# Optimization experiments

Hardware: AMD Instinct MI355X
Metric: run time of the kernel (lower is better)

The kernel has to match this reference:

```python
import jax, jax.numpy as jnp
import numpy as np

N, E, F_IN, H, OUT, G = 40000, 640000, 128, 128, 10, 256


def setup_inputs() -> dict:
    key = jax.random.key(0)
    ks = jax.random.split(key, 8)
    x = jax.random.normal(ks[0], (N, F_IN), dtype=jnp.float32)
    edge_index = jax.random.randint(ks[1], (2, E), 0, N, dtype=jnp.int32)
    batch = jnp.sort(jax.random.randint(ks[2], (N,), 0, G, dtype=jnp.int32))
    W1 = jax.random.normal(ks[3], (F_IN, H), dtype=jnp.float32) / np.sqrt(F_IN)
    b1 = jnp.zeros((H,), dtype=jnp.float32)
    W2 = jax.random.normal(ks[4], (H, H), dtype=jnp.float32) / np.sqrt(H)
    b2 = jnp.zeros((H,), dtype=jnp.float32)
    Wfc = jax.random.normal(ks[5], (H, OUT), dtype=jnp.float32) / np.sqrt(H)
    bfc = jnp.zeros((OUT,), dtype=jnp.float32)
    return {"x": x, "edge_index": edge_index, "batch": batch,
            "W1": W1, "b1": b1, "W2": W2, "b2": b2, "Wfc": Wfc, "bfc": bfc}


def _gcn_conv(x, W, b, row, col, num_nodes):
    # x' = D^{-1/2} (A+I) D^{-1/2} (x W) + b   (self-loops already in row/col)
    xw = x @ W                                            # [N, H]
    ones = jnp.ones(row.shape[0], dtype=x.dtype)
    deg = jax.ops.segment_sum(ones, col, num_segments=num_nodes)
    dinv = jnp.where(deg > 0, jax.lax.rsqrt(jnp.maximum(deg, 1.0)), 0.0)
    norm = dinv[row] * dinv[col]                          # [E+N]
    msg = xw[row] * norm[:, None]                         # gather + scale
    return jax.ops.segment_sum(msg, col, num_segments=num_nodes) + b


def reference(x, edge_index, batch, W1, b1, W2, b2, Wfc, bfc):
    num_nodes = x.shape[0]
    loop = jnp.arange(num_nodes, dtype=edge_index.dtype)
    row = jnp.concatenate([edge_index[0], loop])
    col = jnp.concatenate([edge_index[1], loop])

    h = jax.nn.relu(_gcn_conv(x, W1, b1, row, col, num_nodes))
    h = jax.nn.relu(_gcn_conv(h, W2, b2, row, col, num_nodes))

    # global_mean_pool over graph ids
    sums = jax.ops.segment_sum(h, batch, num_segments=G)  # [G, H]
    cnt = jax.ops.segment_sum(jnp.ones(num_nodes, h.dtype), batch, num_segments=G)
    pooled = sums / jnp.maximum(cnt, 1.0)[:, None]

    logits = pooled @ Wfc + bfc                           # [G, OUT]
    return jax.nn.log_softmax(logits, axis=-1)
```

## Files before the change

### kernel.cpp

```cpp
#include <hip/hip_runtime.h>
#include <math.h>

#define H_DIM 128
#define OUT_DIM 10

typedef __attribute__((ext_vector_type(8))) __bf16 bf16x8;
typedef __attribute__((ext_vector_type(8))) unsigned short ushort8;
typedef __attribute__((ext_vector_type(4))) float f32x4;

__device__ inline unsigned short f2bf_rne(float f) {
    unsigned int u = __float_as_uint(f);
    unsigned int r = u + 0x7FFFu + ((u >> 16) & 1u);
    return (unsigned short)(r >> 16);
}
__device__ inline float bf_lo(unsigned int u) { return __uint_as_float(u << 16); }
__device__ inline float bf_hi(unsigned int u) { return __uint_as_float(u & 0xFFFF0000u); }

__global__ __launch_bounds__(256) void hist_kernel(const int* __restrict__ col,
                                                   int* __restrict__ cnt, int E) {
    int e = blockIdx.x * 256 + threadIdx.x;
    if (e < E) atomicAdd(&cnt[col[e]], 1);
}

__global__ __launch_bounds__(256) void scan_phase1(const int* __restrict__ cnt,
                                                   int* __restrict__ blockSums,
                                                   float* __restrict__ dinv, int N) {
    __shared__ int red[256];
    int base = blockIdx.x * 1024;
    int t = threadIdx.x;
    int s = 0;
    for (int i = 0; i < 4; ++i) {
        int idx = base + t * 4 + i;
        if (idx < N) {
            int cv = cnt[idx];
            s += cv;
            dinv[idx] = rsqrtf((float)cv + 1.0f);
        }
    }
    red[t] = s;
    __syncthreads();
    for (int d = 128; d > 0; d >>= 1) {
        if (t < d) red[t] += red[t + d];
        __syncthreads();
    }
    if (t == 0) blockSums[blockIdx.x] = red[0];
}

__global__ __launch_bounds__(256) void scan_phase2(const int* __restrict__ blockSums,
                                                   int* __restrict__ blockOffs,
                                                   int* __restrict__ offs, int B, int N) {
    __shared__ int sh[256];
    int t = threadIdx.x;
    sh[t] = (t < B) ? blockSums[t] : 0;
    __syncthreads();
    for (int d = 1; d < 256; d <<= 1) {
        int v = (t >= d) ? sh[t - d] : 0;
        __syncthreads();
        sh[t] += v;
        __syncthreads();
    }
    if (t < B) blockOffs[t] = (t == 0) ? 0 : sh[t - 1];
    if (t == 255) offs[N] = sh[255];
}

__global__ __launch_bounds__(256) void scan_phase3(const int* __restrict__ cnt,
                                                   const int* __restrict__ blockOffs,
                                                   int* __restrict__ offs,
                                                   int* __restrict__ cursor, int N) {
    __shared__ int red[256];
    int base = blockIdx.x * 1024;
    int t = threadIdx.x;
    int v[4];
    int s = 0;
    for (int i = 0; i < 4; ++i) {
        int idx = base + t * 4 + i;
        v[i] = (idx < N) ? cnt[idx] : 0;
        s += v[i];
    }
    red[t] = s;
    __syncthreads();
    for (int d = 1; d < 256; d <<= 1) {
        int x = (t >= d) ? red[t - d] : 0;
        __syncthreads();
        red[t] += x;
        __syncthreads();
    }
    int run = blockOffs[blockIdx.x] + ((t == 0) ? 0 : red[t - 1]);
    for (int i = 0; i < 4; ++i) {
        int idx = base + t * 4 + i;
        if (idx < N) { offs[idx] = run; cursor[idx] = run; run += v[i]; }
    }
}

__global__ __launch_bounds__(256) void scatter_kernel(const int* __restrict__ row,
                                                      const int* __restrict__ col,
                                                      const float* __restrict__ dinv,
                                                      int* __restrict__ cursor,
                                                      int2* __restrict__ csr, int E) {
    int e = blockIdx.x * 256 + threadIdx.x;
    if (e >= E) return;
    int r = row[e], c = col[e];
    int pos = atomicAdd(&cursor[c], 1);
    int2 p; p.x = r; p.y = __float_as_int(dinv[r] * dinv[c]);
    csr[pos] = p;
}

__global__ __launch_bounds__(256) void wconvert(const float* __restrict__ W1,
                                                const float* __restrict__ W2,
                                                unsigned short* __restrict__ Wt1Hi,
                                                unsigned short* __restrict__ Wt1Lo,
                                                unsigned short* __restrict__ Wt2Hi,
                                                unsigned short* __restrict__ Wt2Lo) {
    int i = blockIdx.x * 256 + threadIdx.x;
    const float* src       = (i < 16384) ? W1    : W2;
    unsigned short* dh     = (i < 16384) ? Wt1Hi : Wt2Hi;
    unsigned short* dl     = (i < 16384) ? Wt1Lo : Wt2Lo;
    int idx = i & 16383;
    int k = idx >> 7, n = idx & 127;
    float v = src[idx];
    unsigned short hb = f2bf_rne(v);
    float hf = __uint_as_float((unsigned int)hb << 16);
    unsigned short lb = f2bf_rne(v - hf);
    dh[n * H_DIM + k] = hb;
    dl[n * H_DIM + k] = lb;
}

__global__ __launch_bounds__(256) void xsplit(const float* __restrict__ X,
                                              unsigned short* __restrict__ Xhi,
                                              unsigned short* __restrict__ Xlo,
                                              int total8) {
    int i = blockIdx.x * 256 + threadIdx.x;
    if (i >= total8) return;
    const float* p = X + (size_t)i * 8;
    f32x4 a = *(const f32x4*)p;
    f32x4 b = *(const f32x4*)(p + 4);
    float v[8] = {a.x, a.y, a.z, a.w, b.x, b.y, b.z, b.w};
    ushort8 h, l;
    #pragma unroll
    for (int j = 0; j < 8; ++j) {
        unsigned short hb = f2bf_rne(v[j]);
        float hf = __uint_as_float((unsigned int)hb << 16);
        h[j] = hb;
        l[j] = f2bf_rne(v[j] - hf);
    }
    *(ushort8*)(Xhi + (size_t)i * 8) = h;
    *(ushort8*)(Xlo + (size_t)i * 8) = l;
}

__global__ __launch_bounds__(256) void gemm_mfma_splitA(const unsigned short* __restrict__ Ahi,
                                                        const unsigned short* __restrict__ Alo,
                                                        const unsigned short* __restrict__ WtHi,
                                                        const unsigned short* __restrict__ WtLo,
                                                        unsigned short* __restrict__ Yb, int N) {
    int lane = threadIdx.x & 63;
    int wv   = threadIdx.x >> 6;
    int m16  = lane & 15;
    int quad = lane >> 4;
    int nodeBase = blockIdx.x * 32;

    f32x4 acc[2][2] = {};

    #pragma unroll
    for (int kt = 0; kt < 4; ++kt) {
        int k0 = kt * 32 + quad * 8;

        ushort8 aHi[2], aLo[2];
        #pragma unroll
        for (int mi = 0; mi < 2; ++mi) {
            int node = nodeBase + mi * 16 + m16;
            if (node >= N) node = N - 1;
            size_t off = (size_t)node * H_DIM + k0;
            aHi[mi] = *(const ushort8*)(Ahi + off);
            aLo[mi] = *(const ushort8*)(Alo + off);
        }

        ushort8 bHi[2], bLo[2];
        #pragma unroll
        for (int ni = 0; ni < 2; ++ni) {
            int n = (wv * 2 + ni) * 16 + m16;
            size_t off = (size_t)n * H_DIM + k0;
            bHi[ni] = *(const ushort8*)(WtHi + off);
            bLo[ni] = *(const ushort8*)(WtLo + off);
        }

        #pragma unroll
        for (int mi = 0; mi < 2; ++mi)
            #pragma unroll
            for (int ni = 0; ni < 2; ++ni) {
                acc[mi][ni] = __builtin_amdgcn_mfma_f32_16x16x32_bf16(
                    __builtin_bit_cast(bf16x8, aHi[mi]),
                    __builtin_bit_cast(bf16x8, bHi[ni]), acc[mi][ni], 0, 0, 0);
                acc[mi][ni] = __builtin_amdgcn_mfma_f32_16x16x32_bf16(
                    __builtin_bit_cast(bf16x8, aLo[mi]),
                    __builtin_bit_cast(bf16x8, bHi[ni]), acc[mi][ni], 0, 0, 0);
                acc[mi][ni] = __builtin_amdgcn_mfma_f32_16x16x32_bf16(
                    __builtin_bit_cast(bf16x8, aHi[mi]),
                    __builtin_bit_cast(bf16x8, bLo[ni]), acc[mi][ni], 0, 0, 0);
            }
    }

    #pragma unroll
    for (int mi = 0; mi < 2; ++mi)
        #pragma unroll
        for (int r = 0; r < 4; ++r) {
            int node = nodeBase + mi * 16 + quad * 4 + r;
            if (node < N) {
                #pragma unroll
                for (int ni = 0; ni < 2; ++ni) {
                    int c = (wv * 2 + ni) * 16 + m16;
                    Yb[(size_t)node * H_DIM + c] = f2bf_rne(acc[mi][ni][r]);
                }
            }
        }
}

__global__ __launch_bounds__(256) void gemm_mfma_bf16A(const unsigned short* __restrict__ Xb,
                                                       const unsigned short* __restrict__ WtHi,
                                                       const unsigned short* __restrict__ WtLo,
                                                       unsigned short* __restrict__ Yb, int N) {
    int lane = threadIdx.x & 63;
    int wv   = threadIdx.x >> 6;
    int m16  = lane & 15;
    int quad = lane >> 4;
    int nodeBase = blockIdx.x * 32;

    f32x4 acc[2][2] = {};

    #pragma unroll
    for (int kt = 0; kt < 4; ++kt) {
        int k0 = kt * 32 + quad * 8;

        ushort8 a[2];
        #pragma unroll
        for (int mi = 0; mi < 2; ++mi) {
            int node = nodeBase + mi * 16 + m16;
            if (node >= N) node = N - 1;
            a[mi] = *(const ushort8*)(Xb + (size_t)node * H_DIM + k0);
        }

        ushort8 bHi[2], bLo[2];
        #pragma unroll
        for (int ni = 0; ni < 2; ++ni) {
            int n = (wv * 2 + ni) * 16 + m16;
            size_t off = (size_t)n * H_DIM + k0;
            bHi[ni] = *(const ushort8*)(WtHi + off);
            bLo[ni] = *(const ushort8*)(WtLo + off);
        }

        #pragma unroll
        for (int mi = 0; mi < 2; ++mi)
            #pragma unroll
            for (int ni = 0; ni < 2; ++ni) {
                acc[mi][ni] = __builtin_amdgcn_mfma_f32_16x16x32_bf16(
                    __builtin_bit_cast(bf16x8, a[mi]),
                    __builtin_bit_cast(bf16x8, bHi[ni]), acc[mi][ni], 0, 0, 0);
                acc[mi][ni] = __builtin_amdgcn_mfma_f32_16x16x32_bf16(
                    __builtin_bit_cast(bf16x8, a[mi]),
                    __builtin_bit_cast(bf16x8, bLo[ni]), acc[mi][ni], 0, 0, 0);
            }
    }

    #pragma unroll
    for (int mi = 0; mi < 2; ++mi)
        #pragma unroll
        for (int r = 0; r < 4; ++r) {
            int node = nodeBase + mi * 16 + quad * 4 + r;
            if (node < N) {
                #pragma unroll
                for (int ni = 0; ni < 2; ++ni) {
                    int c = (wv * 2 + ni) * 16 + m16;
                    Yb[(size_t)node * H_DIM + c] = f2bf_rne(acc[mi][ni][r]);
                }
            }
        }
}

__global__ __launch_bounds__(256) void agg_fused(const unsigned short* __restrict__ XWb,
                                                 const float* __restrict__ dinv,
                                                 const int2* __restrict__ csr,
                                                 const int* __restrict__ offs,
                                                 const float* __restrict__ bias,
                                                 unsigned short* __restrict__ OUTb, int N) {
    int wave = (blockIdx.x * 256 + threadIdx.x) >> 6;
    int lane = threadIdx.x & 63;
    if (wave >= N) return;
    int c = wave;
    int start = offs[c], end = offs[c + 1];
    float dc = dinv[c];
    const unsigned int* XW32 = (const unsigned int*)XWb;

    float ax0, ay0;
    {
        unsigned int u = XW32[(size_t)c * 64 + lane];
        float s = dc * dc;
        ax0 = bf_lo(u) * s; ay0 = bf_hi(u) * s;
    }
    float ax1 = 0.f, ay1 = 0.f, ax2 = 0.f, ay2 = 0.f, ax3 = 0.f, ay3 = 0.f;

    for (int base = start; base < end; base += 64) {
        int m = end - base; if (m > 64) m = 64;
        int2 ce; ce.x = 0; ce.y = 0;
        if (lane < m) ce = csr[base + lane];

        int j = 0;
        for (; j + 3 < m; j += 4) {
            int r0 = __shfl(ce.x, j);     int b0 = __shfl(ce.y, j);
            int r1 = __shfl(ce.x, j + 1); int b1 = __shfl(ce.y, j + 1);
            int r2 = __shfl(ce.x, j + 2); int b2 = __shfl(ce.y, j + 2);
            int r3 = __shfl(ce.x, j + 3); int b3 = __shfl(ce.y, j + 3);
            unsigned int g0 = XW32[(size_t)r0 * 64 + lane];
            unsigned int g1 = XW32[(size_t)r1 * 64 + lane];
            unsigned int g2 = XW32[(size_t)r2 * 64 + lane];
            unsigned int g3 = XW32[(size_t)r3 * 64 + lane];
            float n0 = __int_as_float(b0);
            float n1 = __int_as_float(b1);
            float n2 = __int_as_float(b2);
            float n3 = __int_as_float(b3);
            ax0 += bf_lo(g0) * n0; ay0 += bf_hi(g0) * n0;
            ax1 += bf_lo(g1) * n1; ay1 += bf_hi(g1) * n1;
            ax2 += bf_lo(g2) * n2; ay2 += bf_hi(g2) * n2;
            ax3 += bf_lo(g3) * n3; ay3 += bf_hi(g3) * n3;
        }
        for (; j < m; ++j) {
            int r = __shfl(ce.x, j); int b = __shfl(ce.y, j);
            unsigned int g = XW32[(size_t)r * 64 + lane];
            float nrm = __int_as_float(b);
            ax1 += bf_lo(g) * nrm; ay1 += bf_hi(g) * nrm;
        }
    }
    float ax = (ax0 + ax1) + (ax2 + ax3);
    float ay = (ay0 + ay1) + (ay2 + ay3);
    float2 b = ((const float2*)bias)[lane];
    ax = fmaxf(ax + b.x, 0.f);
    ay = fmaxf(ay + b.y, 0.f);
    unsigned int o = (unsigned int)f2bf_rne(ax) | ((unsigned int)f2bf_rne(ay) << 16);
    ((unsigned int*)(OUTb + (size_t)c * H_DIM))[lane] = o;
}

__global__ __launch_bounds__(256) void pool_partial(const unsigned short* __restrict__ Hb,
                                                    const int* __restrict__ batch,
                                                    float* __restrict__ pooledSum, int N) {
    __shared__ int sb[64];
    int base = blockIdx.x * 64;
    int t = threadIdx.x;
    if (t < 64) {
        int idx = base + t;
        sb[t] = (idx < N) ? batch[idx] : -1;
    }
    __syncthreads();
    int f   = t & 127;
    int sub = t >> 7;
    int n0  = sub * 32;
    float acc = 0.f;
    int curg = -1;
    #pragma unroll 4
    for (int i = 0; i < 32; ++i) {
        int n = base + n0 + i;
        if (n >= N) break;
        int g = sb[n0 + i];
        if (g != curg) {
            if (curg >= 0) atomicAdd(&pooledSum[curg * H_DIM + f], acc);
            acc = 0.f; curg = g;
        }
        acc += __uint_as_float(((unsigned int)Hb[(size_t)n * H_DIM + f]) << 16);
    }
    if (curg >= 0) atomicAdd(&pooledSum[curg * H_DIM + f], acc);
}

__global__ __launch_bounds__(64) void head_kernel(const float* __restrict__ pooledSum,
                                                  const int* __restrict__ batch,
                                                  const float* __restrict__ Wfc,
                                                  const float* __restrict__ bfc,
                                                  float* __restrict__ out, int N) {
    __shared__ float sl[OUT_DIM + 2];
    __shared__ int bounds[2];
    int g = blockIdx.x;
    int j = threadIdx.x;
    if (j < 2) {
        int v = g + j;
        int lo = 0, hi = N;
        while (lo < hi) {
            int mid = (lo + hi) >> 1;
            if (batch[mid] < v) lo = mid + 1; else hi = mid;
        }
        bounds[j] = lo;
    }
    __syncthreads();
    int cnt = bounds[1] - bounds[0];
    float inv = 1.0f / (float)(cnt > 0 ? cnt : 1);
    if (j < OUT_DIM) {
        float acc = 0.f;
        const float* p = pooledSum + g * H_DIM;
        for (int k = 0; k < H_DIM; ++k) acc += p[k] * Wfc[k * OUT_DIM + j];
        sl[j] = acc * inv + bfc[j];
    }
    __syncthreads();
    if (j == 0) {
        float m = sl[0];
        for (int i = 1; i < OUT_DIM; ++i) m = fmaxf(m, sl[i]);
        float s = 0.f;
        for (int i = 0; i < OUT_DIM; ++i) s += expf(sl[i] - m);
        sl[OUT_DIM] = m + logf(s);
    }
    __syncthreads();
    if (j < OUT_DIM) out[g * OUT_DIM + j] = sl[j] - sl[OUT_DIM];
}

extern "C" void kernel_launch(void* const* d_in, const int* in_sizes, int n_in,
                              void* d_out, int out_size, void* d_ws, size_t ws_size,
                              hipStream_t stream) {
    const float* x     = (const float*)d_in[0];
    const int*   ei    = (const int*)  d_in[1];
    const int*   batch = (const int*)  d_in[2];
    const float* W1    = (const float*)d_in[3];
    const float* b1    = (const float*)d_in[4];
    const float* W2    = (const float*)d_in[5];
    const float* b2    = (const float*)d_in[6];
    const float* Wfc   = (const float*)d_in[7];
    const float* bfc   = (const float*)d_in[8];
    float* out = (float*)d_out;

    int N = in_sizes[2];
    int E = in_sizes[1] / 2;
    int G = out_size / OUT_DIM;
    const int* row = ei;
    const int* col = ei + E;

    char* wsb = (char*)d_ws;
    size_t nAlign = (size_t)((N + 256) / 256) * 256;
    int*   cnt    = (int*)wsb;
    int*   offs   = cnt + nAlign;
    int*   cursor = offs + nAlign;
    float* dinv   = (float*)(cursor + nAlign);
    int2*  csr    = (int2*)(dinv + nAlign);
    unsigned short* Xb = (unsigned short*)(csr + E);
    unsigned short* Hb = Xb + (size_t)N * H_DIM;
    float* pooledSum = (float*)(Hb + (size_t)N * H_DIM);
    int* blockSums = (int*)(pooledSum + (size_t)G * H_DIM);
    int* blockOffs = blockSums + 256;
    unsigned short* Wt1Hi = (unsigned short*)(blockOffs + 256);
    unsigned short* Wt1Lo = Wt1Hi + H_DIM * H_DIM;
    unsigned short* Wt2Hi = Wt1Lo + H_DIM * H_DIM;
    unsigned short* Wt2Lo = Wt2Hi + H_DIM * H_DIM;
    unsigned short* Xhi = Wt2Lo + H_DIM * H_DIM;
    unsigned short* Xlo = Xhi + (size_t)N * H_DIM;

    int scanBlocks = (N + 1023) / 1024;
    int total8 = N * H_DIM / 8;

    wconvert<<<128, 256, 0, stream>>>(W1, W2, Wt1Hi, Wt1Lo, Wt2Hi, Wt2Lo);
    xsplit<<<(total8 + 255) / 256, 256, 0, stream>>>(x, Xhi, Xlo, total8);

    hipMemsetAsync(cnt, 0, N * sizeof(int), stream);
    hist_kernel<<<(E + 255) / 256, 256, 0, stream>>>(col, cnt, E);
    scan_phase1<<<scanBlocks, 256, 0, stream>>>(cnt, blockSums, dinv, N);
    scan_phase2<<<1, 256, 0, stream>>>(blockSums, blockOffs, offs, scanBlocks, N);
    scan_phase3<<<scanBlocks, 256, 0, stream>>>(cnt, blockOffs, offs, cursor, N);
    scatter_kernel<<<(E + 255) / 256, 256, 0, stream>>>(row, col, dinv, cursor, csr, E);

    int aggBlocks  = (N + 3) / 4;
    int gemmBlocks = (N + 31) / 32;

    gemm_mfma_splitA<<<gemmBlocks, 256, 0, stream>>>(Xhi, Xlo, Wt1Hi, Wt1Lo, Xb, N);
    agg_fused<<<aggBlocks, 256, 0, stream>>>(Xb, dinv, csr, offs, b1, Hb, N);

    gemm_mfma_bf16A<<<gemmBlocks, 256, 0, stream>>>(Hb, Wt2Hi, Wt2Lo, Xb, N);
    agg_fused<<<aggBlocks, 256, 0, stream>>>(Xb, dinv, csr, offs, b2, Hb, N);

    hipMemsetAsync(pooledSum, 0, (size_t)G * H_DIM * sizeof(float), stream);
    pool_partial<<<(N + 63) / 64, 256, 0, stream>>>(Hb, batch, pooledSum, N);
    head_kernel<<<G, 64, 0, stream>>>(pooledSum, batch, Wfc, bfc, out, N);
}
```

Baseline: 273.6 us.

## Fuse prep kernels, use single-pass decoupled scan, merge memsets

Merges the weight conversion, x hi/lo split and degree histogram into one launch with block-range dispatch. Replaces the three-phase scan with a single-pass chained scan where each block waits on its predecessor's flag. Rearranges the workspace so one memset clears the counts, the pool accumulators and the scan flags. This removes several kernel launches and inter-kernel gaps. It adds a serial spin-wait chain across the roughly 40 scan blocks, which relies on earlier blocks being scheduled first.

```diff
diff --git a/kernel.cpp b/kernel.cpp
--- a/kernel.cpp
+++ b/kernel.cpp
@@ -16,66 +16,77 @@
 __device__ inline float bf_lo(unsigned int u) { return __uint_as_float(u << 16); }
 __device__ inline float bf_hi(unsigned int u) { return __uint_as_float(u & 0xFFFF0000u); }
 
-__global__ __launch_bounds__(256) void hist_kernel(const int* __restrict__ col,
+__global__ __launch_bounds__(256) void prep_kernel(const float* __restrict__ W1,
+                                                   const float* __restrict__ W2,
+                                                   unsigned short* __restrict__ Wt1Hi,
+                                                   unsigned short* __restrict__ Wt1Lo,
+                                                   unsigned short* __restrict__ Wt2Hi,
+                                                   unsigned short* __restrict__ Wt2Lo,
+                                                   const float* __restrict__ X,
+                                                   unsigned short* __restrict__ Xhi,
+                                                   unsigned short* __restrict__ Xlo,
+                                                   int total8, int xb,
+                                                   const int* __restrict__ col,
                                                    int* __restrict__ cnt, int E) {
-    int e = blockIdx.x * 256 + threadIdx.x;
-    if (e < E) atomicAdd(&cnt[col[e]], 1);
-}
-
-__global__ __launch_bounds__(256) void scan_phase1(const int* __restrict__ cnt,
-                                                   int* __restrict__ blockSums,
-                                                   float* __restrict__ dinv, int N) {
+    if (blockIdx.x < 128) {
+        int i = blockIdx.x * 256 + threadIdx.x;
+        const float* src   = (i < 16384) ? W1    : W2;
+        unsigned short* dh = (i < 16384) ? Wt1Hi : Wt2Hi;
+        unsigned short* dl = (i < 16384) ? Wt1Lo : Wt2Lo;
+        int idx = i & 16383;
+        int k = idx >> 7, n = idx & 127;
+        float v = src[idx];
+        unsigned short hb = f2bf_rne(v);
+        float hf = __uint_as_float((unsigned int)hb << 16);
+        unsigned short lb = f2bf_rne(v - hf);
+        dh[n * H_DIM + k] = hb;
+        dl[n * H_DIM + k] = lb;
+    } else if (blockIdx.x < 128 + xb) {
+        int i = (blockIdx.x - 128) * 256 + threadIdx.x;
+        if (i >= total8) return;
+        const float* p = X + (size_t)i * 8;
+        f32x4 a = *(const f32x4*)p;
+        f32x4 b = *(const f32x4*)(p + 4);
+        float v[8] = {a.x, a.y, a.z, a.w, b.x, b.y, b.z, b.w};
+        ushort8 h, l;
+        #pragma unroll
+        for (int j = 0; j < 8; ++j) {
+            unsigned short hb = f2bf_rne(v[j]);
+            float hf = __uint_as_float((unsigned int)hb << 16);
+            h[j] = hb;
+            l[j] = f2bf_rne(v[j] - hf);
+        }
+        *(ushort8*)(Xhi + (size_t)i * 8) = h;
+        *(ushort8*)(Xlo + (size_t)i * 8) = l;
+    } else {
+        int e = (blockIdx.x - 128 - xb) * 256 + threadIdx.x;
+        if (e < E) atomicAdd(&cnt[col[e]], 1);
+    }
+}
+
+__global__ __launch_bounds__(256) void scan_onepass(const int* __restrict__ cnt,
+                                                    int* __restrict__ offs,
+                                                    int* __restrict__ cursor,
+                                                    float* __restrict__ dinv,
+                                                    int* __restrict__ flags,
+                                                    int* __restrict__ incl,
+                                                    int N, int B) {
     __shared__ int red[256];
-    int base = blockIdx.x * 1024;
+    __shared__ int sPrev;
+    int bid = blockIdx.x;
+    int base = bid * 1024;
     int t = threadIdx.x;
+    int v[4];
     int s = 0;
+    #pragma unroll
     for (int i = 0; i < 4; ++i) {
         int idx = base + t * 4 + i;
         if (idx < N) {
             int cv = cnt[idx];
+            v[i] = cv;
             s += cv;
             dinv[idx] = rsqrtf((float)cv + 1.0f);
-        }
-    }
-    red[t] = s;
-    __syncthreads();
-    for (int d = 128; d > 0; d >>= 1) {
-        if (t < d) red[t] += red[t + d];
-        __syncthreads();
-    }
-    if (t == 0) blockSums[blockIdx.x] = red[0];
-}
-
-__global__ __launch_bounds__(256) void scan_phase2(const int* __restrict__ blockSums,
-                                                   int* __restrict__ blockOffs,
-                                                   int* __restrict__ offs, int B, int N) {
-    __shared__ int sh[256];
-    int t = threadIdx.x;
-    sh[t] = (t < B) ? blockSums[t] : 0;
-    __syncthreads();
-    for (int d = 1; d < 256; d <<= 1) {
-        int v = (t >= d) ? sh[t - d] : 0;
-        __syncthreads();
-        sh[t] += v;
-        __syncthreads();
-    }
-    if (t < B) blockOffs[t] = (t == 0) ? 0 : sh[t - 1];
-    if (t == 255) offs[N] = sh[255];
-}
-
-__global__ __launch_bounds__(256) void scan_phase3(const int* __restrict__ cnt,
-                                                   const int* __restrict__ blockOffs,
-                                                   int* __restrict__ offs,
-                                                   int* __restrict__ cursor, int N) {
-    __shared__ int red[256];
-    int base = blockIdx.x * 1024;
-    int t = threadIdx.x;
-    int v[4];
-    int s = 0;
-    for (int i = 0; i < 4; ++i) {
-        int idx = base + t * 4 + i;
-        v[i] = (idx < N) ? cnt[idx] : 0;
-        s += v[i];
+        } else v[i] = 0;
     }
     red[t] = s;
     __syncthreads();
@@ -85,11 +96,26 @@
         red[t] += x;
         __syncthreads();
     }
-    int run = blockOffs[blockIdx.x] + ((t == 0) ? 0 : red[t - 1]);
+    if (t == 0) {
+        int blockTotal = red[255];
+        int prev = 0;
+        if (bid > 0) {
+            while (atomicAdd(&flags[bid - 1], 0) == 0) { }
+            prev = atomicAdd(&incl[bid - 1], 0);
+        }
+        atomicExch(&incl[bid], prev + blockTotal);
+        __threadfence();
+        atomicExch(&flags[bid], 1);
+        sPrev = prev;
+    }
+    __syncthreads();
+    int run = sPrev + ((t == 0) ? 0 : red[t - 1]);
+    #pragma unroll
     for (int i = 0; i < 4; ++i) {
         int idx = base + t * 4 + i;
         if (idx < N) { offs[idx] = run; cursor[idx] = run; run += v[i]; }
     }
+    if (bid == B - 1 && t == 255) offs[N] = run;
 }
 
 __global__ __launch_bounds__(256) void scatter_kernel(const int* __restrict__ row,
@@ -103,48 +129,6 @@
     int pos = atomicAdd(&cursor[c], 1);
     int2 p; p.x = r; p.y = __float_as_int(dinv[r] * dinv[c]);
     csr[pos] = p;
-}
-
-__global__ __launch_bounds__(256) void wconvert(const float* __restrict__ W1,
-                                                const float* __restrict__ W2,
-                                                unsigned short* __restrict__ Wt1Hi,
-                                                unsigned short* __restrict__ Wt1Lo,
-                                                unsigned short* __restrict__ Wt2Hi,
-                                                unsigned short* __restrict__ Wt2Lo) {
-    int i = blockIdx.x * 256 + threadIdx.x;
-    const float* src       = (i < 16384) ? W1    : W2;
-    unsigned short* dh     = (i < 16384) ? Wt1Hi : Wt2Hi;
-    unsigned short* dl     = (i < 16384) ? Wt1Lo : Wt2Lo;
-    int idx = i & 16383;
-    int k = idx >> 7, n = idx & 127;
-    float v = src[idx];
-    unsigned short hb = f2bf_rne(v);
-    float hf = __uint_as_float((unsigned int)hb << 16);
-    unsigned short lb = f2bf_rne(v - hf);
-    dh[n * H_DIM + k] = hb;
-    dl[n * H_DIM + k] = lb;
-}
-
-__global__ __launch_bounds__(256) void xsplit(const float* __restrict__ X,
-                                              unsigned short* __restrict__ Xhi,
-                                              unsigned short* __restrict__ Xlo,
-                                              int total8) {
-    int i = blockIdx.x * 256 + threadIdx.x;
-    if (i >= total8) return;
-    const float* p = X + (size_t)i * 8;
-    f32x4 a = *(const f32x4*)p;
-    f32x4 b = *(const f32x4*)(p + 4);
-    float v[8] = {a.x, a.y, a.z, a.w, b.x, b.y, b.z, b.w};
-    ushort8 h, l;
-    #pragma unroll
-    for (int j = 0; j < 8; ++j) {
-        unsigned short hb = f2bf_rne(v[j]);
-        float hf = __uint_as_float((unsigned int)hb << 16);
-        h[j] = hb;
-        l[j] = f2bf_rne(v[j] - hf);
-    }
-    *(ushort8*)(Xhi + (size_t)i * 8) = h;
-    *(ushort8*)(Xlo + (size_t)i * 8) = l;
 }
 
 __global__ __launch_bounds__(256) void gemm_mfma_splitA(const unsigned short* __restrict__ Ahi,
@@ -428,17 +412,17 @@
 
     char* wsb = (char*)d_ws;
     size_t nAlign = (size_t)((N + 256) / 256) * 256;
-    int*   cnt    = (int*)wsb;
-    int*   offs   = cnt + nAlign;
-    int*   cursor = offs + nAlign;
-    float* dinv   = (float*)(cursor + nAlign);
-    int2*  csr    = (int2*)(dinv + nAlign);
+    int*   cnt       = (int*)wsb;
+    float* pooledSum = (float*)(cnt + nAlign);
+    int*   scanFlags = (int*)(pooledSum + (size_t)G * H_DIM);
+    int*   scanIncl  = scanFlags + 64;
+    int*   offs      = scanIncl + 64;
+    int*   cursor    = offs + nAlign;
+    float* dinv      = (float*)(cursor + nAlign);
+    int2*  csr       = (int2*)(dinv + nAlign);
     unsigned short* Xb = (unsigned short*)(csr + E);
     unsigned short* Hb = Xb + (size_t)N * H_DIM;
-    float* pooledSum = (float*)(Hb + (size_t)N * H_DIM);
-    int* blockSums = (int*)(pooledSum + (size_t)G * H_DIM);
-    int* blockOffs = blockSums + 256;
-    unsigned short* Wt1Hi = (unsigned short*)(blockOffs + 256);
+    unsigned short* Wt1Hi = Hb + (size_t)N * H_DIM;
     unsigned short* Wt1Lo = Wt1Hi + H_DIM * H_DIM;
     unsigned short* Wt2Hi = Wt1Lo + H_DIM * H_DIM;
     unsigned short* Wt2Lo = Wt2Hi + H_DIM * H_DIM;
@@ -447,15 +431,16 @@
 
     int scanBlocks = (N + 1023) / 1024;
     int total8 = N * H_DIM / 8;
-
-    wconvert<<<128, 256, 0, stream>>>(W1, W2, Wt1Hi, Wt1Lo, Wt2Hi, Wt2Lo);
-    xsplit<<<(total8 + 255) / 256, 256, 0, stream>>>(x, Xhi, Xlo, total8);
-
-    hipMemsetAsync(cnt, 0, N * sizeof(int), stream);
-    hist_kernel<<<(E + 255) / 256, 256, 0, stream>>>(col, cnt, E);
-    scan_phase1<<<scanBlocks, 256, 0, stream>>>(cnt, blockSums, dinv, N);
-    scan_phase2<<<1, 256, 0, stream>>>(blockSums, blockOffs, offs, scanBlocks, N);
-    scan_phase3<<<scanBlocks, 256, 0, stream>>>(cnt, blockOffs, offs, cursor, N);
+    int xb = (total8 + 255) / 256;
+    int histBlocks = (E + 255) / 256;
+
+    hipMemsetAsync(cnt, 0, (nAlign + (size_t)G * H_DIM + 128) * sizeof(int), stream);
+
+    prep_kernel<<<128 + xb + histBlocks, 256, 0, stream>>>(
+        W1, W2, Wt1Hi, Wt1Lo, Wt2Hi, Wt2Lo, x, Xhi, Xlo, total8, xb, col, cnt, E);
+
+    scan_onepass<<<scanBlocks, 256, 0, stream>>>(cnt, offs, cursor, dinv,
+                                                 scanFlags, scanIncl, N, scanBlocks);
     scatter_kernel<<<(E + 255) / 256, 256, 0, stream>>>(row, col, dinv, cursor, csr, E);
 
     int aggBlocks  = (N + 3) / 4;
@@ -467,7 +452,6 @@
     gemm_mfma_bf16A<<<gemmBlocks, 256, 0, stream>>>(Hb, Wt2Hi, Wt2Lo, Xb, N);
     agg_fused<<<aggBlocks, 256, 0, stream>>>(Xb, dinv, csr, offs, b2, Hb, N);
 
-    hipMemsetAsync(pooledSum, 0, (size_t)G * H_DIM * sizeof(float), stream);
     pool_partial<<<(N + 63) / 64, 256, 0, stream>>>(Hb, batch, pooledSum, N);
     head_kernel<<<G, 64, 0, stream>>>(pooledSum, batch, Wfc, bfc, out, N);
 }
```

After: 311.8 us. +14.0%, slower.
